# Kernel tuning notes

Hardware: AMD Instinct MI355X
Metric: run time of the kernel (lower is better)

The kernel has to match this reference:

```python
import jax, jax.numpy as jnp
import numpy as np

GAMMA = 0.5
BATCH, DIM, UNITS = 16384, 512, 1024


def setup_inputs() -> dict:
    key = jax.random.key(0)
    k1, k2 = jax.random.split(key)
    inputs = jax.random.normal(k1, (BATCH, DIM), dtype=jnp.float32)
    mu = jax.random.normal(k2, (DIM, UNITS), dtype=jnp.float32)
    return {"inputs": inputs, "mu": mu}


def reference(inputs, mu):
    # Squared L2 distance from each input row to each center (column of mu):
    x_sq = jnp.sum(inputs * inputs, axis=1, keepdims=True)        # [B, 1]
    mu_sq = jnp.sum(mu * mu, axis=0, keepdims=True)               # [1, U]
    cross = inputs @ mu                                           # [B, U] GEMM
    l2 = x_sq - 2.0 * cross + mu_sq                                # [B, U]
    return jnp.exp(-GAMMA * l2)
```

## Files before the change

### kernel.cpp

```cpp
#include <hip/hip_runtime.h>
#include <hip/hip_bf16.h>

#define BATCH 16384
#define DIM   512
#define UNITS 1024

typedef float v16f __attribute__((ext_vector_type(16)));

#define APITCH 516
#define BPITCH 33

__device__ __forceinline__ void async_copy16(const void* g, void* l) {
    __builtin_amdgcn_global_load_lds(
        (const __attribute__((address_space(1))) void*)g,
        (__attribute__((address_space(3))) void*)l,
        16 , 0 , 0 );
}

__global__ __launch_bounds__(256)
void prep_kernel(const float* __restrict__ in, const float* __restrict__ mu,
                 unsigned char* __restrict__ A8f, unsigned char* __restrict__ B8f,
                 float* __restrict__ xsq, float* __restrict__ musq) {
    __shared__ __attribute__((aligned(16))) char smem[512 * BPITCH * 4 + 1024];
    const int t  = threadIdx.x;
    const int l  = t & 63, w = t >> 6;
    const int ln = l & 31, h = l >> 5;

    if (blockIdx.x >= UNITS / 32) {
        float* lds = (float*)smem;
        float* red = (float*)(smem + 32 * APITCH * 4);
        const int bb = blockIdx.x - UNITS / 32;
        const int c  = (bb & 7) * 64 + (bb >> 3);
        const float4* src = (const float4*)(in + (size_t)c * 32 * DIM);
        float4* l4 = (float4*)lds;
#pragma unroll
        for (int i = 0; i < 16; i++) {
            const int f = i * 256 + t;
            l4[(f >> 7) * (APITCH / 4) + (f & 127)] = src[f];
        }
        __syncthreads();
        float s = 0.f;
#pragma unroll
        for (int j = 0; j < 8; j++) {
            const int kw = w * 8 + j;
            const float* p = lds + ln * APITCH + kw * 16 + h * 8;
            float4 f0 = *(const float4*)p;
            float4 f1 = *(const float4*)(p + 4);
            s += f0.x * f0.x + f0.y * f0.y + f0.z * f0.z + f0.w * f0.w
               + f1.x * f1.x + f1.y * f1.y + f1.z * f1.z + f1.w * f1.w;
            int lo = __builtin_amdgcn_cvt_pk_fp8_f32(f0.x, f0.y, 0, false);
            lo     = __builtin_amdgcn_cvt_pk_fp8_f32(f0.z, f0.w, lo, true);
            int hi = __builtin_amdgcn_cvt_pk_fp8_f32(f1.x, f1.y, 0, false);
            hi     = __builtin_amdgcn_cvt_pk_fp8_f32(f1.z, f1.w, hi, true);
            *(int2*)(A8f + (((size_t)c * 32 + kw) * 64 + l) * 8) = make_int2(lo, hi);
        }
        red[ln * 8 + w * 2 + h] = s;
        __syncthreads();
        if (t < 32) {
            float a = 0.f;
#pragma unroll
            for (int i = 0; i < 8; i++) a += red[t * 8 + i];
            xsq[c * 32 + t] = a;
        }
    } else {
        float* lds = (float*)smem;
        float* red = (float*)(smem + 512 * BPITCH * 4);
        const int nb = blockIdx.x;
        const int n0 = nb * 32;
        const int col = t & 31, kg = t >> 5;
        float s = 0.f;
        for (int i = 0; i < 64; i++) {
            const int k = i * 8 + kg;
            float v = mu[(size_t)k * UNITS + n0 + col];
            s += v * v;
            lds[k * BPITCH + col] = v;
        }
        red[col * 8 + kg] = s;
        __syncthreads();
        if (t < 32) {
            float a = 0.f;
#pragma unroll
            for (int i = 0; i < 8; i++) a += red[t * 8 + i];
            musq[n0 + t] = a;
        }
#pragma unroll
        for (int j = 0; j < 8; j++) {
            const int kw = w * 8 + j;
            const float* p = lds + (kw * 16 + h * 8) * BPITCH + ln;
            float f[8];
#pragma unroll
            for (int i = 0; i < 8; i++) f[i] = p[i * BPITCH];
            int lo = __builtin_amdgcn_cvt_pk_fp8_f32(f[0], f[1], 0, false);
            lo     = __builtin_amdgcn_cvt_pk_fp8_f32(f[2], f[3], lo, true);
            int hi = __builtin_amdgcn_cvt_pk_fp8_f32(f[4], f[5], 0, false);
            hi     = __builtin_amdgcn_cvt_pk_fp8_f32(f[6], f[7], hi, true);
            *(int2*)(B8f + (((size_t)nb * 32 + kw) * 64 + l) * 8) = make_int2(lo, hi);
        }
    }
}

__global__ __launch_bounds__(1024, 4)
void rbf_gemm_kernel(const unsigned char* __restrict__ A8f,
                     const unsigned char* __restrict__ B8f,
                     const float* __restrict__ xsq,
                     const float* __restrict__ musq,
                     float* __restrict__ out) {
    __shared__ __attribute__((aligned(16))) unsigned char Bs[131072];

    const int t  = threadIdx.x;
    const int l  = t & 63;
    const int w  = t >> 6;
    const int ln = l & 31;
    const int h  = l >> 5;

    const int b  = blockIdx.x;
    const int x  = b & 7;
    const int j  = b >> 3;
    const int mt = x * 8 + (j & 7);
    const int nt = j >> 3;
    const int m0 = mt * 256;
    const int n0 = nt * 256;
    const int wm = (w >> 2) * 64;
    const int wn = (w & 3) * 64;

    const unsigned char* bsrc = B8f + (size_t)n0 * 512;
#pragma unroll
    for (int i = 0; i < 8; i++) {
        const int c = i * 1024 + t;
        async_copy16(bsrc + c * 16, Bs + c * 16);
    }
    __syncthreads();

    const long* Af  = (const long*)A8f + (size_t)((m0 + wm) >> 5) * 2048 + l;
    const long* lbp = (const long*)Bs + (size_t)(wn >> 5) * 2048 + l;

    v16f acc[2][2];
#pragma unroll
    for (int c = 0; c < 2; c++)
#pragma unroll
        for (int g = 0; g < 2; g++) acc[c][g] = (v16f)0.f;

#pragma unroll 4
    for (int kw = 0; kw < 32; kw++) {
        long a0 = Af[kw * 64];
        long a1 = Af[2048 + kw * 64];
        long b0 = lbp[kw * 64];
        long b1 = lbp[2048 + kw * 64];
        acc[0][0] = __builtin_amdgcn_mfma_f32_32x32x16_fp8_fp8(a0, b0, acc[0][0], 0, 0, 0);
        acc[0][1] = __builtin_amdgcn_mfma_f32_32x32x16_fp8_fp8(a0, b1, acc[0][1], 0, 0, 0);
        acc[1][0] = __builtin_amdgcn_mfma_f32_32x32x16_fp8_fp8(a1, b0, acc[1][0], 0, 0, 0);
        acc[1][1] = __builtin_amdgcn_mfma_f32_32x32x16_fp8_fp8(a1, b1, acc[1][1], 0, 0, 0);
    }

#pragma unroll
    for (int c = 0; c < 2; c++) {
        const int mc = m0 + wm + c * 32;
        const float xv = -0.5f * xsq[mc + ln];
#pragma unroll
        for (int g = 0; g < 2; g++) {
            const int nc = n0 + wn + g * 32;
            const float mb = -0.5f * musq[nc + ln];
#pragma unroll
            for (int r = 0; r < 16; r++) {
                const int rl = (r & 3) + 8 * (r >> 2) + 4 * h;
                const float xb = __shfl(xv, rl, 64);
                float v = __expf(acc[c][g][r] + xb + mb);
                __builtin_nontemporal_store(
                    v, out + (size_t)(mc + rl) * UNITS + nc + ln);
            }
        }
    }
}

extern "C" void kernel_launch(void* const* d_in, const int* in_sizes, int n_in,
                              void* d_out, int out_size, void* d_ws, size_t ws_size,
                              hipStream_t stream) {
    const float* inputs = (const float*)d_in[0];
    const float* mu     = (const float*)d_in[1];
    float* out = (float*)d_out;

    char* ws = (char*)d_ws;
    unsigned char* A8f = (unsigned char*)ws;
    unsigned char* B8f = (unsigned char*)(ws + (size_t)BATCH * DIM);
    float* xsq  = (float*)(ws + (size_t)BATCH * DIM + (size_t)UNITS * DIM);
    float* musq = xsq + BATCH;

    prep_kernel<<<UNITS / 32 + BATCH / 32, 256, 0, stream>>>(
        inputs, mu, A8f, B8f, xsq, musq);
    rbf_gemm_kernel<<<256, 1024, 0, stream>>>(A8f, B8f, xsq, musq, out);
}
```

Measured before the change: 112.0 us.

## Halve GEMM N-tile to 128 and overlap second-half B staging with compute

The GEMM block moves from a 256x256 tile with 1024 threads to a 256x128 tile with 512 threads, launching 512 blocks and using 64KB of LDS instead of 128KB. B is now staged into LDS in two K-halves: the second half's async copies are issued right after the first barrier, so they overlap with the MFMA loop over the first half. The aim is shorter block startup latency, more resident blocks per CU, and better load balance across CUs. In exchange, each A tile is read from global memory by twice as many blocks, and a block adds an extra barrier.

```diff
diff --git a/kernel.cpp b/kernel.cpp
--- a/kernel.cpp
+++ b/kernel.cpp
@@ -99,13 +99,13 @@
     }
 }
 
-__global__ __launch_bounds__(1024, 4)
+__global__ __launch_bounds__(512, 4)
 void rbf_gemm_kernel(const unsigned char* __restrict__ A8f,
                      const unsigned char* __restrict__ B8f,
                      const float* __restrict__ xsq,
                      const float* __restrict__ musq,
                      float* __restrict__ out) {
-    __shared__ __attribute__((aligned(16))) unsigned char Bs[131072];
+    __shared__ __attribute__((aligned(16))) unsigned char Bs[65536];
 
     const int t  = threadIdx.x;
     const int l  = t & 63;
@@ -119,20 +119,33 @@
     const int mt = x * 8 + (j & 7);
     const int nt = j >> 3;
     const int m0 = mt * 256;
-    const int n0 = nt * 256;
-    const int wm = (w >> 2) * 64;
-    const int wn = (w & 3) * 64;
-
-    const unsigned char* bsrc = B8f + (size_t)n0 * 512;
-#pragma unroll
-    for (int i = 0; i < 8; i++) {
-        const int c = i * 1024 + t;
-        async_copy16(bsrc + c * 16, Bs + c * 16);
-    }
+    const int n0 = nt * 128;
+    const int wm = (w >> 1) * 64;
+    const int wn = (w & 1) * 64;
+    const int ng0 = n0 >> 5;
+
+#define STAGE(hf)                                                           \
+    {                                                                       \
+        _Pragma("unroll")                                                   \
+        for (int i = 0; i < 4; i++) {                                       \
+            const int c   = i * 512 + t;                                    \
+            const int g   = c >> 9;                                         \
+            const int kwl = (c >> 5) & 15;                                  \
+            const int byt = (c & 31) * 16;                                  \
+            async_copy16(                                                   \
+                B8f + ((size_t)(ng0 + g) * 32 + (hf) * 16 + kwl) * 512 + byt, \
+                Bs + ((g * 32 + (hf) * 16 + kwl) * 512 + byt));             \
+        }                                                                   \
+    }
+
+    STAGE(0);
     __syncthreads();
-
-    const long* Af  = (const long*)A8f + (size_t)((m0 + wm) >> 5) * 2048 + l;
-    const long* lbp = (const long*)Bs + (size_t)(wn >> 5) * 2048 + l;
+    STAGE(1);
+
+    const long* Af0 = (const long*)(A8f + (size_t)((m0 + wm) >> 5) * 16384) + l;
+    const long* Af1 = Af0 + 2048;
+    const long* Bl0 = (const long*)(Bs + (wn >> 5) * 16384) + l;
+    const long* Bl1 = Bl0 + 2048;
 
     v16f acc[2][2];
 #pragma unroll
@@ -141,11 +154,23 @@
         for (int g = 0; g < 2; g++) acc[c][g] = (v16f)0.f;
 
 #pragma unroll 4
-    for (int kw = 0; kw < 32; kw++) {
-        long a0 = Af[kw * 64];
-        long a1 = Af[2048 + kw * 64];
-        long b0 = lbp[kw * 64];
-        long b1 = lbp[2048 + kw * 64];
+    for (int kw = 0; kw < 16; kw++) {
+        long a0 = Af0[kw * 64];
+        long a1 = Af1[kw * 64];
+        long b0 = Bl0[kw * 64];
+        long b1 = Bl1[kw * 64];
+        acc[0][0] = __builtin_amdgcn_mfma_f32_32x32x16_fp8_fp8(a0, b0, acc[0][0], 0, 0, 0);
+        acc[0][1] = __builtin_amdgcn_mfma_f32_32x32x16_fp8_fp8(a0, b1, acc[0][1], 0, 0, 0);
+        acc[1][0] = __builtin_amdgcn_mfma_f32_32x32x16_fp8_fp8(a1, b0, acc[1][0], 0, 0, 0);
+        acc[1][1] = __builtin_amdgcn_mfma_f32_32x32x16_fp8_fp8(a1, b1, acc[1][1], 0, 0, 0);
+    }
+    __syncthreads();
+#pragma unroll 4
+    for (int kw = 16; kw < 32; kw++) {
+        long a0 = Af0[kw * 64];
+        long a1 = Af1[kw * 64];
+        long b0 = Bl0[kw * 64];
+        long b1 = Bl1[kw * 64];
         acc[0][0] = __builtin_amdgcn_mfma_f32_32x32x16_fp8_fp8(a0, b0, acc[0][0], 0, 0, 0);
         acc[0][1] = __builtin_amdgcn_mfma_f32_32x32x16_fp8_fp8(a0, b1, acc[0][1], 0, 0, 0);
         acc[1][0] = __builtin_amdgcn_mfma_f32_32x32x16_fp8_fp8(a1, b0, acc[1][0], 0, 0, 0);
@@ -170,6 +195,7 @@
             }
         }
     }
+#undef STAGE
 }
 
 extern "C" void kernel_launch(void* const* d_in, const int* in_sizes, int n_in,
@@ -187,5 +213,5 @@
 
     prep_kernel<<<UNITS / 32 + BATCH / 32, 256, 0, stream>>>(
         inputs, mu, A8f, B8f, xsq, musq);
-    rbf_gemm_kernel<<<256, 1024, 0, stream>>>(A8f, B8f, xsq, musq, out);
-}
+    rbf_gemm_kernel<<<512, 512, 0, stream>>>(A8f, B8f, xsq, musq, out);
+}
```

Result: slower. 115.5 us (+3.2%).
